# Performance work log

Hardware: AMD Instinct MI355X
Metric: run time of the kernel (lower is better)

The kernel has to match this reference:

```python
import jax, jax.numpy as jnp
import numpy as np

B, C, T = 16, 256, 2048
K = 1024  # codes per layer
N_LAYERS = 3


def setup_inputs() -> dict:
    key = jax.random.key(0)
    kx, k0, k1, k2 = jax.random.split(key, 4)
    x = jax.random.normal(kx, (B, C, T), dtype=jnp.float32)
    scale = 1.0 / K
    emb0 = jax.random.uniform(k0, (K, C), minval=-scale, maxval=scale, dtype=jnp.float32)
    emb1 = jax.random.uniform(k1, (K, C), minval=-scale, maxval=scale, dtype=jnp.float32)
    emb2 = jax.random.uniform(k2, (K, C), minval=-scale, maxval=scale, dtype=jnp.float32)
    return {"x": x, "emb0": emb0, "emb1": emb1, "emb2": emb2}


def _vq_layer(x, emb):
    # x: [B, C, T], emb: [K, C]
    b, c, t = x.shape
    flat = jnp.transpose(x, (0, 2, 1)).reshape(-1, c)          # [B*T, C]
    # squared L2 distance to each code: ||f||^2 - 2 f.e + ||e||^2
    dist = (jnp.sum(flat * flat, axis=1, keepdims=True)
            - 2.0 * flat @ emb.T
            + jnp.sum(emb * emb, axis=1))                       # [B*T, K]
    idx = jnp.argmin(dist, axis=1)                              # [B*T]
    quant = jnp.transpose(emb[idx].reshape(b, t, c), (0, 2, 1)) # [B, C, T]
    sg = jax.lax.stop_gradient
    loss = jnp.mean((sg(quant) - x) ** 2) + jnp.mean((quant - sg(x)) ** 2)
    quantized = x + sg(quant - x)  # straight-through
    return quantized, loss


def reference(x, emb0, emb1, emb2):
    total_loss = jnp.float32(0.0)
    out = x
    for emb in (emb0, emb1, emb2):
        out, loss = _vq_layer(out, emb)
        total_loss = total_loss + loss
    return out, total_loss
```

## Files before the change

### kernel.cpp

```cpp
#include <hip/hip_runtime.h>
#include <stdint.h>

#define B_  16
#define C_  256
#define T_  2048
#define K_  1024
#define TOTAL_ELEMS 8388608

typedef short bf16x8 __attribute__((ext_vector_type(8)));
typedef float f32x4 __attribute__((ext_vector_type(4)));

__device__ __forceinline__ unsigned long long pack_key(float d, int idx) {
  unsigned u = __float_as_uint(d);
  u = (u & 0x80000000u) ? ~u : (u | 0x80000000u);
  return ((unsigned long long)u << 32) | (unsigned)idx;
}
__device__ __forceinline__ float unpack_dist(unsigned long long key) {
  unsigned du = (unsigned)(key >> 32);
  unsigned bits = (du & 0x80000000u) ? (du ^ 0x80000000u) : ~du;
  return __uint_as_float(bits);
}

__device__ __forceinline__ unsigned short f2bf_rne(float f) {
  unsigned u = __float_as_uint(f);
  unsigned r = u + 0x7FFFu + ((u >> 16) & 1u);
  return (unsigned short)(r >> 16);
}

__global__ __launch_bounds__(256) void prep_kernel(
    const float* __restrict__ e0, const float* __restrict__ e1,
    const float* __restrict__ e2, float* __restrict__ nrm,
    unsigned short* __restrict__ ebt, uint4* __restrict__ keys_region,
    float* __restrict__ loss_accum, unsigned* __restrict__ counter) {
  int bid = blockIdx.x;
  int tid = threadIdx.x;
  if (bid < 12) {
    int i = bid * 256 + tid;
    const float* e = (i < 1024) ? e0 : (i < 2048) ? e1 : e2;
    const float* p = e + (size_t)(i & 1023) * C_;
    float s = 0.0f;
    for (int c = 0; c < C_; c += 4) {
      float4 v = *(const float4*)(p + c);
      s = fmaf(v.x, v.x, s); s = fmaf(v.y, v.y, s);
      s = fmaf(v.z, v.z, s); s = fmaf(v.w, v.w, s);
    }
    nrm[i] = s;
  } else if (bid < 268) {
    int code = (bid - 12) * 4 + (tid >> 6);
    int c = (tid & 63) * 4;
    float4 v = *(const float4*)(e0 + (size_t)code * C_ + c);
    unsigned lo = (unsigned)f2bf_rne(v.x) | ((unsigned)f2bf_rne(v.y) << 16);
    unsigned hi = (unsigned)f2bf_rne(v.z) | ((unsigned)f2bf_rne(v.w) << 16);
    int kk = c >> 5, lg = (c >> 3) & 3, j = c & 7;
    *(uint2*)(ebt + ((size_t)(kk * 1024 + code) * 4 + lg) * 8 + j) = make_uint2(lo, hi);
  } else {
    int i = (bid - 268) * 256 + tid;
    keys_region[i] = make_uint4(0xFFFFFFFFu, 0xFFFFFFFFu, 0xFFFFFFFFu, 0xFFFFFFFFu);
    if (bid == 268 && tid == 0) { *loss_accum = 0.0f; *counter = 0u; }
  }
}

__global__ __launch_bounds__(256) void map_tile_kernel(
    const float* __restrict__ e0, const float* __restrict__ e1,
    const float* __restrict__ e2, const float* __restrict__ nrm,
    unsigned long long* __restrict__ keysM) {
  __shared__ float As[16][68];
  __shared__ float Bs[16][68];
  int bid = blockIdx.x;
  int m = bid >> 8;
  int tb = bid & 255;
  int ar0 = (tb >> 4) << 6;
  int br0 = (tb & 15) << 6;
  const float* Ap = m ? e1 : e0;
  const float* Bp = m ? e2 : e1;
  const float* nB = nrm + (m + 1) * 1024;

  int tid = threadIdx.x;
  int ty = tid >> 4, tx = tid & 15;
  int srow = tid >> 2;
  int skp  = (tid & 3) << 2;

  float acc[4][4];
#pragma unroll
  for (int i = 0; i < 4; i++)
#pragma unroll
    for (int j = 0; j < 4; j++) acc[i][j] = 0.0f;

  const float* gA = Ap + (size_t)(ar0 + srow) * C_ + skp;
  const float* gB = Bp + (size_t)(br0 + srow) * C_ + skp;

  for (int kk = 0; kk < C_; kk += 16) {
    float4 av = *(const float4*)(gA + kk);
    float4 bv = *(const float4*)(gB + kk);
    __syncthreads();
    As[skp + 0][srow] = av.x; As[skp + 1][srow] = av.y;
    As[skp + 2][srow] = av.z; As[skp + 3][srow] = av.w;
    Bs[skp + 0][srow] = bv.x; Bs[skp + 1][srow] = bv.y;
    Bs[skp + 2][srow] = bv.z; Bs[skp + 3][srow] = bv.w;
    __syncthreads();
#pragma unroll
    for (int k = 0; k < 16; k++) {
      float4 a4 = *(const float4*)&As[k][ty * 4];
      float4 b4 = *(const float4*)&Bs[k][tx * 4];
      float aa[4] = {a4.x, a4.y, a4.z, a4.w};
      float bb[4] = {b4.x, b4.y, b4.z, b4.w};
#pragma unroll
      for (int i = 0; i < 4; i++)
#pragma unroll
        for (int j = 0; j < 4; j++)
          acc[i][j] = fmaf(aa[i], bb[j], acc[i][j]);
    }
  }

  float nv[4];
#pragma unroll
  for (int j = 0; j < 4; j++) nv[j] = nB[br0 + tx * 4 + j];

#pragma unroll
  for (int i = 0; i < 4; i++) {
    unsigned long long best = 0xFFFFFFFFFFFFFFFFULL;
#pragma unroll
    for (int j = 0; j < 4; j++) {
      int code = br0 + tx * 4 + j;
      float s = nv[j] - 2.0f * acc[i][j];
      unsigned long long key = pack_key(s, code);
      if (key < best) best = key;
    }
#pragma unroll
    for (int off = 1; off < 16; off <<= 1) {
      unsigned long long o = __shfl_xor(best, off, 64);
      if (o < best) best = o;
    }
    if (tx == 0)
      atomicMin(&keysM[m * 1024 + ar0 + ty * 4 + i], best);
  }
}

__global__ __launch_bounds__(256, 2) void l0_fused_kernel(
    const float* __restrict__ x, const unsigned short* __restrict__ ebt,
    const float* __restrict__ e0n, unsigned long long* __restrict__ keys,
    float* __restrict__ loss_accum) {
  __shared__ __align__(16) char Abuf[32768];
  __shared__ unsigned long long kred[64][4];
  __shared__ float red[4];

  int tid = threadIdx.x;
  int l = tid & 63, w = tid >> 6;
  int lr = l & 15, lg = l >> 4;
  int q  = blockIdx.x >> 9;
  int mb = blockIdx.x & 511;
  int row0 = mb << 6;

  {
    int row = tid & 63;
    int cg  = tid >> 6;
    int bb  = mb >> 5;
    int t0  = (mb & 31) << 6;
    const float* xb = x + (size_t)bb * (C_ * T_) + t0 + row;
    float sumsq = 0.0f;
#pragma unroll
    for (int i = 0; i < 8; i++) {
      int c0 = cg * 64 + i * 8;
      float v[8];
#pragma unroll
      for (int u = 0; u < 8; u++) {
        v[u] = xb[(size_t)(c0 + u) * T_];
        sumsq = fmaf(v[u], v[u], sumsq);
      }
      unsigned pk[4];
#pragma unroll
      for (int j = 0; j < 4; j++)
        pk[j] = (unsigned)f2bf_rne(v[2 * j]) | ((unsigned)f2bf_rne(v[2 * j + 1]) << 16);
      int cc = c0 >> 3;
      *(uint4*)(Abuf + ((size_t)cc * 64 + row) * 16) =
          make_uint4(pk[0], pk[1], pk[2], pk[3]);
    }
    for (int off = 32; off > 0; off >>= 1) sumsq += __shfl_down(sumsq, off, 64);
    if (l == 0) red[w] = sumsq;
  }
  __syncthreads();
  if (q == 0 && tid == 0)
    atomicAdd(loss_accum, red[0] + red[1] + red[2] + red[3]);

  const unsigned short* pB = ebt + ((size_t)((q << 8) + w * 64 + lr) * 4 + lg) * 8;

#define LOADB(s, kk_) do {                                                   \
    const unsigned short* q_ = pB + (size_t)(kk_) * 32768;                   \
    s##0 = *(const bf16x8*)(q_);                                             \
    s##1 = *(const bf16x8*)(q_ + 512);                                       \
    s##2 = *(const bf16x8*)(q_ + 1024);                                      \
    s##3 = *(const bf16x8*)(q_ + 1536);                                      \
  } while (0)

#define DOKK(kk_, s) do {                                                    \
    const char* ab_ = Abuf + (size_t)(((kk_) * 4 + lg) * 64 + lr) * 16;      \
    bf16x8 a0_ = *(const bf16x8*)(ab_);                                      \
    bf16x8 a1_ = *(const bf16x8*)(ab_ + 256);                                \
    bf16x8 a2_ = *(const bf16x8*)(ab_ + 512);                                \
    bf16x8 a3_ = *(const bf16x8*)(ab_ + 768);                                \
    acc[0][0] = __builtin_amdgcn_mfma_f32_16x16x32_bf16(a0_, s##0, acc[0][0], 0, 0, 0); \
    acc[1][0] = __builtin_amdgcn_mfma_f32_16x16x32_bf16(a1_, s##0, acc[1][0], 0, 0, 0); \
    acc[2][0] = __builtin_amdgcn_mfma_f32_16x16x32_bf16(a2_, s##0, acc[2][0], 0, 0, 0); \
    acc[3][0] = __builtin_amdgcn_mfma_f32_16x16x32_bf16(a3_, s##0, acc[3][0], 0, 0, 0); \
    acc[0][1] = __builtin_amdgcn_mfma_f32_16x16x32_bf16(a0_, s##1, acc[0][1], 0, 0, 0); \
    acc[1][1] = __builtin_amdgcn_mfma_f32_16x16x32_bf16(a1_, s##1, acc[1][1], 0, 0, 0); \
    acc[2][1] = __builtin_amdgcn_mfma_f32_16x16x32_bf16(a2_, s##1, acc[2][1], 0, 0, 0); \
    acc[3][1] = __builtin_amdgcn_mfma_f32_16x16x32_bf16(a3_, s##1, acc[3][1], 0, 0, 0); \
    acc[0][2] = __builtin_amdgcn_mfma_f32_16x16x32_bf16(a0_, s##2, acc[0][2], 0, 0, 0); \
    acc[1][2] = __builtin_amdgcn_mfma_f32_16x16x32_bf16(a1_, s##2, acc[1][2], 0, 0, 0); \
    acc[2][2] = __builtin_amdgcn_mfma_f32_16x16x32_bf16(a2_, s##2, acc[2][2], 0, 0, 0); \
    acc[3][2] = __builtin_amdgcn_mfma_f32_16x16x32_bf16(a3_, s##2, acc[3][2], 0, 0, 0); \
    acc[0][3] = __builtin_amdgcn_mfma_f32_16x16x32_bf16(a0_, s##3, acc[0][3], 0, 0, 0); \
    acc[1][3] = __builtin_amdgcn_mfma_f32_16x16x32_bf16(a1_, s##3, acc[1][3], 0, 0, 0); \
    acc[2][3] = __builtin_amdgcn_mfma_f32_16x16x32_bf16(a2_, s##3, acc[2][3], 0, 0, 0); \
    acc[3][3] = __builtin_amdgcn_mfma_f32_16x16x32_bf16(a3_, s##3, acc[3][3], 0, 0, 0); \
  } while (0)

  f32x4 acc[4][4];
#pragma unroll
  for (int ni = 0; ni < 4; ni++) {
    float iv = -0.5f * e0n[(q << 8) + w * 64 + ni * 16 + lr];
    f32x4 ivv = {iv, iv, iv, iv};
#pragma unroll
    for (int mi = 0; mi < 4; mi++) acc[mi][ni] = ivv;
  }

  bf16x8 bA0, bA1, bA2, bA3, bB0, bB1, bB2, bB3;
  LOADB(bA, 0);
  LOADB(bB, 1); DOKK(0, bA);
  LOADB(bA, 2); DOKK(1, bB);
  LOADB(bB, 3); DOKK(2, bA);
  LOADB(bA, 4); DOKK(3, bB);
  LOADB(bB, 5); DOKK(4, bA);
  LOADB(bA, 6); DOKK(5, bB);
  LOADB(bB, 7); DOKK(6, bA);
  DOKK(7, bB);
#undef LOADB
#undef DOKK

#pragma unroll
  for (int mi = 0; mi < 4; mi++) {
#pragma unroll
    for (int r = 0; r < 4; r++) {
      unsigned long long best = 0xFFFFFFFFFFFFFFFFULL;
#pragma unroll
      for (int ni = 0; ni < 4; ni++) {
        int code = (q << 8) | (w << 6) | (ni << 4) | lr;
        unsigned long long key = pack_key(-2.0f * acc[mi][ni][r], code);
        if (key < best) best = key;
      }
#pragma unroll
      for (int off = 1; off < 16; off <<= 1) {
        unsigned long long o = __shfl_xor(best, off, 64);
        if (o < best) best = o;
      }
      if (lr == 0) kred[mi * 16 + lg * 4 + r][w] = best;
    }
  }
  __syncthreads();
  if (tid < 64) {
    unsigned long long b0 = kred[tid][0], b1 = kred[tid][1];
    unsigned long long b2 = kred[tid][2], b3 = kred[tid][3];
    if (b1 < b0) b0 = b1;
    if (b3 < b2) b2 = b3;
    atomicMin(&keys[row0 + tid], b0 < b2 ? b0 : b2);
  }
}

__global__ __launch_bounds__(256) void finish_kernel(
    const float* __restrict__ emb2,
    const unsigned long long* __restrict__ keys,
    const unsigned long long* __restrict__ keysM,
    const float* __restrict__ nrm,
    float* __restrict__ out, float* __restrict__ loss_accum,
    unsigned* __restrict__ counter) {
  __shared__ int code2_l[64];
  __shared__ float rloss[64];
  int tid = threadIdx.x;
  int b  = blockIdx.x >> 5;
  int t0 = (blockIdx.x & 31) << 6;
  int tt = tid & 63, w = tid >> 6;

  if (w == 0) {
    unsigned long long key0 = keys[(size_t)b * T_ + t0 + tt];
    int idx0 = (int)(key0 & 0xFFFFFFFFULL);
    float s0 = unpack_dist(key0);
    unsigned long long k1 = keysM[idx0];
    int c1 = (int)(k1 & 0xFFFFFFFFULL);
    unsigned long long k2 = keysM[1024 + c1];
    code2_l[tt] = (int)(k2 & 0xFFFFFFFFULL);
    rloss[tt] = s0 + nrm[idx0] + unpack_dist(k1) + nrm[1024 + c1] + unpack_dist(k2);
  }
  __syncthreads();

  float* ob = out + ((size_t)b << 19);
  int code2 = code2_l[tt];
  const float* e2row = emb2 + (size_t)code2 * C_;
  for (int c4 = w * 64; c4 < w * 64 + 64; c4 += 4) {
    float4 ev = *(const float4*)(e2row + c4);
    float evv[4] = {ev.x, ev.y, ev.z, ev.w};
#pragma unroll
    for (int u = 0; u < 4; u++)
      __builtin_nontemporal_store(evv[u], ob + (size_t)(c4 + u) * T_ + t0 + tt);
  }
  if (w == 0) {
    float tot = rloss[tt];
    for (int off = 32; off > 0; off >>= 1)
      tot += __shfl_down(tot, off, 64);
    if (tt == 0) atomicAdd(loss_accum, tot);
  }
  if (tid == 0) {
    __threadfence();
    unsigned old = atomicAdd(counter, 1u);
    if (old == 511u) {
      float L = atomicAdd(loss_accum, 0.0f);
      out[TOTAL_ELEMS] = 2.0f * L / 8388608.0f;
    }
  }
}

extern "C" void kernel_launch(void* const* d_in, const int* in_sizes, int n_in,
                              void* d_out, int out_size, void* d_ws, size_t ws_size,
                              hipStream_t stream) {
  const float* x  = (const float*)d_in[0];
  const float* e0 = (const float*)d_in[1];
  const float* e1 = (const float*)d_in[2];
  const float* e2 = (const float*)d_in[3];
  float* out = (float*)d_out;
  char* ws = (char*)d_ws;

  unsigned long long* keys  = (unsigned long long*)ws;
  unsigned long long* keysM = (unsigned long long*)(ws + 262144);
  float* nrm  = (float*)(ws + 278528);
  float* loss_accum = (float*)(ws + 290816);
  unsigned* counter = (unsigned*)(ws + 290820);
  unsigned short* ebt = (unsigned short*)(ws + 294912);

  prep_kernel<<<336, 256, 0, stream>>>(e0, e1, e2, nrm, ebt, (uint4*)ws,
                                       loss_accum, counter);
  l0_fused_kernel<<<2048, 256, 0, stream>>>(x, ebt, nrm, keys, loss_accum);
  map_tile_kernel<<<512, 256, 0, stream>>>(e0, e1, e2, nrm, keysM);
  finish_kernel<<<512, 256, 0, stream>>>(e2, keys, keysM, nrm, out, loss_accum, counter);
}
```

Measured before the change: 108.0 us.

## Pre-transpose x to bf16 once in prep and merge map kernel into l0

After: 98.64 us. 1.09x faster.

```diff
diff --git a/kernel.cpp b/kernel.cpp
--- a/kernel.cpp
+++ b/kernel.cpp
@@ -27,11 +27,21 @@
   return (unsigned short)(r >> 16);
 }
 
-__global__ __launch_bounds__(256) void prep_kernel(
-    const float* __restrict__ e0, const float* __restrict__ e1,
-    const float* __restrict__ e2, float* __restrict__ nrm,
-    unsigned short* __restrict__ ebt, uint4* __restrict__ keys_region,
-    float* __restrict__ loss_accum, unsigned* __restrict__ counter) {
+__device__ __forceinline__ void gload_lds16(const void* g, void* l) {
+  __builtin_amdgcn_global_load_lds(
+      (const __attribute__((address_space(1))) unsigned int*)g,
+      (__attribute__((address_space(3))) unsigned int*)l, 16, 0, 0);
+}
+
+__global__ __launch_bounds__(256) void prep_xpose_kernel(
+    const float* __restrict__ x, const float* __restrict__ e0,
+    const float* __restrict__ e1, const float* __restrict__ e2,
+    float* __restrict__ nrm, unsigned short* __restrict__ ebt,
+    unsigned short* __restrict__ xTf, uint4* __restrict__ keys_region,
+    float* __restrict__ lossP, float* __restrict__ loss_accum,
+    unsigned* __restrict__ counter) {
+  __shared__ float ftile[64][68];
+  __shared__ float red4[4];
   int bid = blockIdx.x;
   int tid = threadIdx.x;
   if (bid < 12) {
@@ -53,136 +63,78 @@
     unsigned hi = (unsigned)f2bf_rne(v.z) | ((unsigned)f2bf_rne(v.w) << 16);
     int kk = c >> 5, lg = (c >> 3) & 3, j = c & 7;
     *(uint2*)(ebt + ((size_t)(kk * 1024 + code) * 4 + lg) * 8 + j) = make_uint2(lo, hi);
-  } else {
+  } else if (bid < 336) {
     int i = (bid - 268) * 256 + tid;
     keys_region[i] = make_uint4(0xFFFFFFFFu, 0xFFFFFFFFu, 0xFFFFFFFFu, 0xFFFFFFFFu);
     if (bid == 268 && tid == 0) { *loss_accum = 0.0f; *counter = 0u; }
-  }
-}
-
-__global__ __launch_bounds__(256) void map_tile_kernel(
+  } else {
+    int bx = bid - 336;
+    int b  = bx >> 7;
+    int t0 = ((bx >> 2) & 31) << 6;
+    int c0 = (bx & 3) << 6;
+    int cr = tid >> 4;
+    int t_loc = (tid & 15) * 4;
+    const float* src = x + (size_t)b * (C_ * T_) + (size_t)c0 * T_ + t0;
+    float sq = 0.0f;
+#pragma unroll
+    for (int qq = 0; qq < 4; qq++) {
+      int c_loc = cr + qq * 16;
+      float4 v = *(const float4*)(src + (size_t)c_loc * T_ + t_loc);
+      *(float4*)&ftile[c_loc][t_loc] = v;
+      sq = fmaf(v.x, v.x, sq); sq = fmaf(v.y, v.y, sq);
+      sq = fmaf(v.z, v.z, sq); sq = fmaf(v.w, v.w, sq);
+    }
+    for (int off = 32; off > 0; off >>= 1) sq += __shfl_down(sq, off, 64);
+    if ((tid & 63) == 0) red4[tid >> 6] = sq;
+    __syncthreads();
+    if (tid == 0) lossP[bx] = red4[0] + red4[1] + red4[2] + red4[3];
+
+    int t_row = tid >> 2;
+    int cs = (tid & 3) * 16;
+    unsigned pk[8];
+#pragma unroll
+    for (int i = 0; i < 8; i++) {
+      unsigned short lo = f2bf_rne(ftile[cs + 2 * i][t_row]);
+      unsigned short hi = f2bf_rne(ftile[cs + 2 * i + 1][t_row]);
+      pk[i] = (unsigned)lo | ((unsigned)hi << 16);
+    }
+    int mb = b * 32 + (t0 >> 6);
+    int kk = (c0 + cs) >> 5, lg0 = ((c0 + cs) >> 3) & 3;
+    unsigned short* dst = xTf + (size_t)mb * 16384 +
+                          ((size_t)(kk * 4 + lg0) * 64 + t_row) * 8;
+    *(uint4*)dst         = make_uint4(pk[0], pk[1], pk[2], pk[3]);
+    *(uint4*)(dst + 512) = make_uint4(pk[4], pk[5], pk[6], pk[7]);
+  }
+}
+
+__global__ __launch_bounds__(256, 2) void l0map_kernel(
+    const unsigned short* __restrict__ xTf, const unsigned short* __restrict__ ebt,
     const float* __restrict__ e0, const float* __restrict__ e1,
     const float* __restrict__ e2, const float* __restrict__ nrm,
-    unsigned long long* __restrict__ keysM) {
-  __shared__ float As[16][68];
-  __shared__ float Bs[16][68];
+    unsigned long long* __restrict__ keys, unsigned long long* __restrict__ keysM) {
+  __shared__ __align__(16) char smem[34816];
   int bid = blockIdx.x;
-  int m = bid >> 8;
-  int tb = bid & 255;
-  int ar0 = (tb >> 4) << 6;
-  int br0 = (tb & 15) << 6;
-  const float* Ap = m ? e1 : e0;
-  const float* Bp = m ? e2 : e1;
-  const float* nB = nrm + (m + 1) * 1024;
-
   int tid = threadIdx.x;
-  int ty = tid >> 4, tx = tid & 15;
-  int srow = tid >> 2;
-  int skp  = (tid & 3) << 2;
-
-  float acc[4][4];
-#pragma unroll
-  for (int i = 0; i < 4; i++)
-#pragma unroll
-    for (int j = 0; j < 4; j++) acc[i][j] = 0.0f;
-
-  const float* gA = Ap + (size_t)(ar0 + srow) * C_ + skp;
-  const float* gB = Bp + (size_t)(br0 + srow) * C_ + skp;
-
-  for (int kk = 0; kk < C_; kk += 16) {
-    float4 av = *(const float4*)(gA + kk);
-    float4 bv = *(const float4*)(gB + kk);
+
+  if (bid < 2048) {
+    char* Abuf = smem;
+    unsigned long long (*kred)[4] = (unsigned long long(*)[4])(smem + 32768);
+    int l = tid & 63, w = tid >> 6;
+    int lr = l & 15, lg = l >> 4;
+    int q  = bid >> 9;
+    int mb = bid & 511;
+    int row0 = mb << 6;
+
+    {
+      const char* src = (const char*)(xTf + (size_t)mb * 16384);
+      int off = tid * 16;
+#pragma unroll
+      for (int i = 0; i < 8; i++)
+        gload_lds16(src + off + i * 4096, Abuf + off + i * 4096);
+    }
     __syncthreads();
-    As[skp + 0][srow] = av.x; As[skp + 1][srow] = av.y;
-    As[skp + 2][srow] = av.z; As[skp + 3][srow] = av.w;
-    Bs[skp + 0][srow] = bv.x; Bs[skp + 1][srow] = bv.y;
-    Bs[skp + 2][srow] = bv.z; Bs[skp + 3][srow] = bv.w;
-    __syncthreads();
-#pragma unroll
-    for (int k = 0; k < 16; k++) {
-      float4 a4 = *(const float4*)&As[k][ty * 4];
-      float4 b4 = *(const float4*)&Bs[k][tx * 4];
-      float aa[4] = {a4.x, a4.y, a4.z, a4.w};
-      float bb[4] = {b4.x, b4.y, b4.z, b4.w};
-#pragma unroll
-      for (int i = 0; i < 4; i++)
-#pragma unroll
-        for (int j = 0; j < 4; j++)
-          acc[i][j] = fmaf(aa[i], bb[j], acc[i][j]);
-    }
-  }
-
-  float nv[4];
-#pragma unroll
-  for (int j = 0; j < 4; j++) nv[j] = nB[br0 + tx * 4 + j];
-
-#pragma unroll
-  for (int i = 0; i < 4; i++) {
-    unsigned long long best = 0xFFFFFFFFFFFFFFFFULL;
-#pragma unroll
-    for (int j = 0; j < 4; j++) {
-      int code = br0 + tx * 4 + j;
-      float s = nv[j] - 2.0f * acc[i][j];
-      unsigned long long key = pack_key(s, code);
-      if (key < best) best = key;
-    }
-#pragma unroll
-    for (int off = 1; off < 16; off <<= 1) {
-      unsigned long long o = __shfl_xor(best, off, 64);
-      if (o < best) best = o;
-    }
-    if (tx == 0)
-      atomicMin(&keysM[m * 1024 + ar0 + ty * 4 + i], best);
-  }
-}
-
-__global__ __launch_bounds__(256, 2) void l0_fused_kernel(
-    const float* __restrict__ x, const unsigned short* __restrict__ ebt,
-    const float* __restrict__ e0n, unsigned long long* __restrict__ keys,
-    float* __restrict__ loss_accum) {
-  __shared__ __align__(16) char Abuf[32768];
-  __shared__ unsigned long long kred[64][4];
-  __shared__ float red[4];
-
-  int tid = threadIdx.x;
-  int l = tid & 63, w = tid >> 6;
-  int lr = l & 15, lg = l >> 4;
-  int q  = blockIdx.x >> 9;
-  int mb = blockIdx.x & 511;
-  int row0 = mb << 6;
-
-  {
-    int row = tid & 63;
-    int cg  = tid >> 6;
-    int bb  = mb >> 5;
-    int t0  = (mb & 31) << 6;
-    const float* xb = x + (size_t)bb * (C_ * T_) + t0 + row;
-    float sumsq = 0.0f;
-#pragma unroll
-    for (int i = 0; i < 8; i++) {
-      int c0 = cg * 64 + i * 8;
-      float v[8];
-#pragma unroll
-      for (int u = 0; u < 8; u++) {
-        v[u] = xb[(size_t)(c0 + u) * T_];
-        sumsq = fmaf(v[u], v[u], sumsq);
-      }
-      unsigned pk[4];
-#pragma unroll
-      for (int j = 0; j < 4; j++)
-        pk[j] = (unsigned)f2bf_rne(v[2 * j]) | ((unsigned)f2bf_rne(v[2 * j + 1]) << 16);
-      int cc = c0 >> 3;
-      *(uint4*)(Abuf + ((size_t)cc * 64 + row) * 16) =
-          make_uint4(pk[0], pk[1], pk[2], pk[3]);
-    }
-    for (int off = 32; off > 0; off >>= 1) sumsq += __shfl_down(sumsq, off, 64);
-    if (l == 0) red[w] = sumsq;
-  }
-  __syncthreads();
-  if (q == 0 && tid == 0)
-    atomicAdd(loss_accum, red[0] + red[1] + red[2] + red[3]);
-
-  const unsigned short* pB = ebt + ((size_t)((q << 8) + w * 64 + lr) * 4 + lg) * 8;
+
+    const unsigned short* pB = ebt + ((size_t)((q << 8) + w * 64 + lr) * 4 + lg) * 8;
 
 #define LOADB(s, kk_) do {                                                   \
     const unsigned short* q_ = pB + (size_t)(kk_) * 32768;                   \
@@ -216,37 +168,115 @@
     acc[3][3] = __builtin_amdgcn_mfma_f32_16x16x32_bf16(a3_, s##3, acc[3][3], 0, 0, 0); \
   } while (0)
 
-  f32x4 acc[4][4];
-#pragma unroll
-  for (int ni = 0; ni < 4; ni++) {
-    float iv = -0.5f * e0n[(q << 8) + w * 64 + ni * 16 + lr];
-    f32x4 ivv = {iv, iv, iv, iv};
-#pragma unroll
-    for (int mi = 0; mi < 4; mi++) acc[mi][ni] = ivv;
-  }
-
-  bf16x8 bA0, bA1, bA2, bA3, bB0, bB1, bB2, bB3;
-  LOADB(bA, 0);
-  LOADB(bB, 1); DOKK(0, bA);
-  LOADB(bA, 2); DOKK(1, bB);
-  LOADB(bB, 3); DOKK(2, bA);
-  LOADB(bA, 4); DOKK(3, bB);
-  LOADB(bB, 5); DOKK(4, bA);
-  LOADB(bA, 6); DOKK(5, bB);
-  LOADB(bB, 7); DOKK(6, bA);
-  DOKK(7, bB);
+    f32x4 acc[4][4];
+#pragma unroll
+    for (int ni = 0; ni < 4; ni++) {
+      float iv = -0.5f * nrm[(q << 8) + w * 64 + ni * 16 + lr];
+      f32x4 ivv = {iv, iv, iv, iv};
+#pragma unroll
+      for (int mi = 0; mi < 4; mi++) acc[mi][ni] = ivv;
+    }
+
+    bf16x8 bA0, bA1, bA2, bA3, bB0, bB1, bB2, bB3;
+    LOADB(bA, 0);
+    LOADB(bB, 1); DOKK(0, bA);
+    LOADB(bA, 2); DOKK(1, bB);
+    LOADB(bB, 3); DOKK(2, bA);
+    LOADB(bA, 4); DOKK(3, bB);
+    LOADB(bB, 5); DOKK(4, bA);
+    LOADB(bA, 6); DOKK(5, bB);
+    LOADB(bB, 7); DOKK(6, bA);
+    DOKK(7, bB);
 #undef LOADB
 #undef DOKK
 
 #pragma unroll
-  for (int mi = 0; mi < 4; mi++) {
-#pragma unroll
-    for (int r = 0; r < 4; r++) {
+    for (int mi = 0; mi < 4; mi++) {
+#pragma unroll
+      for (int r = 0; r < 4; r++) {
+        unsigned long long best = 0xFFFFFFFFFFFFFFFFULL;
+#pragma unroll
+        for (int ni = 0; ni < 4; ni++) {
+          int code = (q << 8) | (w << 6) | (ni << 4) | lr;
+          unsigned long long key = pack_key(-2.0f * acc[mi][ni][r], code);
+          if (key < best) best = key;
+        }
+#pragma unroll
+        for (int off = 1; off < 16; off <<= 1) {
+          unsigned long long o = __shfl_xor(best, off, 64);
+          if (o < best) best = o;
+        }
+        if (lr == 0) kred[mi * 16 + lg * 4 + r][w] = best;
+      }
+    }
+    __syncthreads();
+    if (tid < 64) {
+      unsigned long long b0 = kred[tid][0], b1 = kred[tid][1];
+      unsigned long long b2 = kred[tid][2], b3 = kred[tid][3];
+      if (b1 < b0) b0 = b1;
+      if (b3 < b2) b2 = b3;
+      atomicMin(&keys[row0 + tid], b0 < b2 ? b0 : b2);
+    }
+  } else {
+    float (*As)[68] = (float(*)[68])smem;
+    float (*Bs)[68] = (float(*)[68])(smem + 4352);
+    int bidm = bid - 2048;
+    int m = bidm >> 8;
+    int tb = bidm & 255;
+    int ar0 = (tb >> 4) << 6;
+    int br0 = (tb & 15) << 6;
+    const float* Ap = m ? e1 : e0;
+    const float* Bp = m ? e2 : e1;
+    const float* nB = nrm + (m + 1) * 1024;
+
+    int ty = tid >> 4, tx = tid & 15;
+    int srow = tid >> 2;
+    int skp  = (tid & 3) << 2;
+
+    float acc[4][4];
+#pragma unroll
+    for (int i = 0; i < 4; i++)
+#pragma unroll
+      for (int j = 0; j < 4; j++) acc[i][j] = 0.0f;
+
+    const float* gA = Ap + (size_t)(ar0 + srow) * C_ + skp;
+    const float* gB = Bp + (size_t)(br0 + srow) * C_ + skp;
+
+    for (int kk = 0; kk < C_; kk += 16) {
+      float4 av = *(const float4*)(gA + kk);
+      float4 bv = *(const float4*)(gB + kk);
+      __syncthreads();
+      As[skp + 0][srow] = av.x; As[skp + 1][srow] = av.y;
+      As[skp + 2][srow] = av.z; As[skp + 3][srow] = av.w;
+      Bs[skp + 0][srow] = bv.x; Bs[skp + 1][srow] = bv.y;
+      Bs[skp + 2][srow] = bv.z; Bs[skp + 3][srow] = bv.w;
+      __syncthreads();
+#pragma unroll
+      for (int k = 0; k < 16; k++) {
+        float4 a4 = *(const float4*)&As[k][ty * 4];
+        float4 b4 = *(const float4*)&Bs[k][tx * 4];
+        float aa[4] = {a4.x, a4.y, a4.z, a4.w};
+        float bb[4] = {b4.x, b4.y, b4.z, b4.w};
+#pragma unroll
+        for (int i = 0; i < 4; i++)
+#pragma unroll
+          for (int j = 0; j < 4; j++)
+            acc[i][j] = fmaf(aa[i], bb[j], acc[i][j]);
+      }
+    }
+
+    float nv[4];
+#pragma unroll
+    for (int j = 0; j < 4; j++) nv[j] = nB[br0 + tx * 4 + j];
+
+#pragma unroll
+    for (int i = 0; i < 4; i++) {
       unsigned long long best = 0xFFFFFFFFFFFFFFFFULL;
 #pragma unroll
-      for (int ni = 0; ni < 4; ni++) {
-        int code = (q << 8) | (w << 6) | (ni << 4) | lr;
-        unsigned long long key = pack_key(-2.0f * acc[mi][ni][r], code);
+      for (int j = 0; j < 4; j++) {
+        int code = br0 + tx * 4 + j;
+        float s = nv[j] - 2.0f * acc[i][j];
+        unsigned long long key = pack_key(s, code);
         if (key < best) best = key;
       }
 #pragma unroll
@@ -254,16 +284,9 @@
         unsigned long long o = __shfl_xor(best, off, 64);
         if (o < best) best = o;
       }
-      if (lr == 0) kred[mi * 16 + lg * 4 + r][w] = best;
-    }
-  }
-  __syncthreads();
-  if (tid < 64) {
-    unsigned long long b0 = kred[tid][0], b1 = kred[tid][1];
-    unsigned long long b2 = kred[tid][2], b3 = kred[tid][3];
-    if (b1 < b0) b0 = b1;
-    if (b3 < b2) b2 = b3;
-    atomicMin(&keys[row0 + tid], b0 < b2 ? b0 : b2);
+      if (tx == 0)
+        atomicMin(&keysM[m * 1024 + ar0 + ty * 4 + i], best);
+    }
   }
 }
 
@@ -271,7 +294,7 @@
     const float* __restrict__ emb2,
     const unsigned long long* __restrict__ keys,
     const unsigned long long* __restrict__ keysM,
-    const float* __restrict__ nrm,
+    const float* __restrict__ nrm, const float* __restrict__ lossP,
     float* __restrict__ out, float* __restrict__ loss_accum,
     unsigned* __restrict__ counter) {
   __shared__ int code2_l[64];
@@ -307,7 +330,11 @@
     float tot = rloss[tt];
     for (int off = 32; off > 0; off >>= 1)
       tot += __shfl_down(tot, off, 64);
-    if (tt == 0) atomicAdd(loss_accum, tot);
+    if (tt == 0) {
+      int j = blockIdx.x * 4;
+      tot += lossP[j] + lossP[j + 1] + lossP[j + 2] + lossP[j + 3];
+      atomicAdd(loss_accum, tot);
+    }
   }
   if (tid == 0) {
     __threadfence();
@@ -334,11 +361,13 @@
   float* nrm  = (float*)(ws + 278528);
   float* loss_accum = (float*)(ws + 290816);
   unsigned* counter = (unsigned*)(ws + 290820);
-  unsigned short* ebt = (unsigned short*)(ws + 294912);
-
-  prep_kernel<<<336, 256, 0, stream>>>(e0, e1, e2, nrm, ebt, (uint4*)ws,
-                                       loss_accum, counter);
-  l0_fused_kernel<<<2048, 256, 0, stream>>>(x, ebt, nrm, keys, loss_accum);
-  map_tile_kernel<<<512, 256, 0, stream>>>(e0, e1, e2, nrm, keysM);
-  finish_kernel<<<512, 256, 0, stream>>>(e2, keys, keysM, nrm, out, loss_accum, counter);
-}
+  float* lossP = (float*)(ws + 290824);
+  unsigned short* ebt = (unsigned short*)(ws + 299520);
+  unsigned short* xTf = (unsigned short*)(ws + 823808);
+
+  prep_xpose_kernel<<<2384, 256, 0, stream>>>(x, e0, e1, e2, nrm, ebt, xTf,
+                                              (uint4*)ws, lossP, loss_accum, counter);
+  l0map_kernel<<<2560, 256, 0, stream>>>(xTf, ebt, e0, e1, e2, nrm, keys, keysM);
+  finish_kernel<<<512, 256, 0, stream>>>(e2, keys, keysM, nrm, lossP, out,
+                                         loss_accum, counter);
+}
```
